# Kernel tuning notes

Hardware: AMD Instinct MI355X
Metric: run time of the kernel (lower is better)

Reference implementation:

```python
import jax, jax.numpy as jnp
import numpy as np

N_NODES = 50000
N_EDGES = 800000
F_IN = 128
HID = 32
HEADS = 8
N_CLS = 2
NEG_SLOPE = 0.2


def _segment_softmax(logits, seg, num_segments):
    # logits: [E, H], seg: [E] destination indices
    m = jax.ops.segment_max(logits, seg, num_segments=num_segments)  # [N, H]
    m = jnp.where(jnp.isfinite(m), m, 0.0)
    e = jnp.exp(logits - m[seg])
    s = jax.ops.segment_sum(e, seg, num_segments=num_segments)  # [N, H]
    return e / (s[seg] + 1e-16)


def _gat_conv(x, src, dst, W, a_src, a_dst, bias, heads, out_ch, concat):
    N = x.shape[0]
    h = (x @ W).reshape(N, heads, out_ch)           # [N, H, C]
    alpha_src = jnp.einsum('nhc,hc->nh', h, a_src)  # [N, H]
    alpha_dst = jnp.einsum('nhc,hc->nh', h, a_dst)  # [N, H]
    logits = jax.nn.leaky_relu(alpha_src[src] + alpha_dst[dst], NEG_SLOPE)  # [E, H]
    alpha = _segment_softmax(logits, dst, N)        # [E, H]
    msg = h[src] * alpha[:, :, None]                # [E, H, C]
    out = jax.ops.segment_sum(msg, dst, num_segments=N)  # [N, H, C]
    out = out.reshape(N, heads * out_ch) if concat else out.mean(axis=1)
    return out + bias


def setup_inputs() -> dict:
    key = jax.random.key(0)
    ks = jax.random.split(key, 12)
    x = jax.random.normal(ks[0], (N_NODES, F_IN), dtype=jnp.float32)
    edge_index = jax.random.randint(ks[1], (2, N_EDGES), 0, N_NODES, dtype=jnp.int32)
    batch = jnp.zeros((N_NODES,), dtype=jnp.int32)
    g1 = 1.0 / np.sqrt(F_IN)
    g2 = 1.0 / np.sqrt(HEADS * HID)
    W1 = jax.random.normal(ks[2], (F_IN, HEADS * HID), dtype=jnp.float32) * g1
    a1_src = jax.random.normal(ks[3], (HEADS, HID), dtype=jnp.float32) * g2
    a1_dst = jax.random.normal(ks[4], (HEADS, HID), dtype=jnp.float32) * g2
    b1 = jnp.zeros((HEADS * HID,), dtype=jnp.float32)
    W2 = jax.random.normal(ks[5], (HEADS * HID, N_CLS), dtype=jnp.float32) * g2
    a2_src = jax.random.normal(ks[6], (1, N_CLS), dtype=jnp.float32)
    a2_dst = jax.random.normal(ks[7], (1, N_CLS), dtype=jnp.float32)
    b2 = jnp.zeros((N_CLS,), dtype=jnp.float32)
    return {"x": x, "edge_index": edge_index, "batch": batch,
            "W1": W1, "a1_src": a1_src, "a1_dst": a1_dst, "b1": b1,
            "W2": W2, "a2_src": a2_src, "a2_dst": a2_dst, "b2": b2}


def reference(x, edge_index, batch, W1, a1_src, a1_dst, b1, W2, a2_src, a2_dst, b2):
    N = x.shape[0]
    # PyG GATConv default add_self_loops=True
    loops = jnp.arange(N, dtype=edge_index.dtype)
    src = jnp.concatenate([edge_index[0], loops])
    dst = jnp.concatenate([edge_index[1], loops])
    # dropout layers are no-ops at inference (training=False)
    h = _gat_conv(x, src, dst, W1, a1_src, a1_dst, b1, HEADS, HID, concat=True)
    h = jax.nn.elu(h)
    out = _gat_conv(h, src, dst, W2, a2_src, a2_dst, b2, 1, N_CLS, concat=False)
    return out
```

## Files before the change

kernel.cpp:

```cpp
#include <hip/hip_runtime.h>

#define NN 50000
#define NP 50048
#define NE 800000
#define ET (NE + NN)
#define NB 196
#define CAP 8192
#define EPB 4096
#define P1_B ((ET + EPB - 1) / EPB)
#define CONVW_B 32
#define CONVX_B (NP * 32 / 1024)
#define FRONT_B (P1_B + CONVW_B + CONVX_B)
#define GEMM_B (NP / 64)
#define MID_B (NB + GEMM_B)

typedef __attribute__((ext_vector_type(8))) short short8;
typedef __attribute__((ext_vector_type(4))) float f32x4;

static __device__ __forceinline__ float bf2f(unsigned short u) {
  union { unsigned int i; float f; } v; v.i = ((unsigned int)u) << 16; return v.f;
}
static __device__ __forceinline__ unsigned short f2bf(float f) {
  union { unsigned int i; float f; } v; v.f = f;
  unsigned int r = v.i + 0x7fffu + ((v.i >> 16) & 1u);
  return (unsigned short)(r >> 16);
}
static __device__ __forceinline__ float lrelu(float z) { return z > 0.f ? z : 0.2f * z; }

__global__ __launch_bounds__(1024) void k_front(
    const int* __restrict__ ei, int* __restrict__ gcount, int* __restrict__ tmp,
    const float* __restrict__ W1, unsigned short* __restrict__ wh,
    const float* __restrict__ x, unsigned short* __restrict__ xh) {
  __shared__ int hist[NB];
  __shared__ int lbase[NB];
  const int b = blockIdx.x;
  const int tid = threadIdx.x;
  if (b < P1_B) {
    if (tid < NB) hist[tid] = 0;
    __syncthreads();
    const int e0 = b * EPB + tid;
    int bkv[4], locv[4], pkv[4];
    bool val[4];
#pragma unroll
    for (int j = 0; j < 4; ++j) {
      int e = e0 + j * 1024;
      val[j] = (e < ET);
      int s = 0, d = 0;
      if (val[j]) {
        s = (e < NE) ? ei[e] : (e - NE);
        d = (e < NE) ? ei[NE + e] : (e - NE);
      }
      bkv[j] = d >> 8;
      pkv[j] = (s << 8) | (d & 255);
      locv[j] = val[j] ? atomicAdd(&hist[bkv[j]], 1) : 0;
    }
    __syncthreads();
    if (tid < NB) {
      int c = hist[tid];
      lbase[tid] = (c > 0) ? atomicAdd(&gcount[tid], c) : 0;
    }
    __syncthreads();
#pragma unroll
    for (int j = 0; j < 4; ++j)
      if (val[j]) tmp[bkv[j] * CAP + lbase[bkv[j]] + locv[j]] = pkv[j];
  } else if (b < P1_B + CONVW_B) {
    int i = (b - P1_B) * 1024 + tid;
    int k = i >> 8, n = i & 255;
    wh[n * 128 + k] = f2bf(W1[i]);
  } else {
    int i4 = (b - P1_B - CONVW_B) * 1024 + tid;
    int i = i4 * 4;
    int row = i >> 7;
    float4 v = (row < NN) ? *(const float4*)(x + i) : (float4){0.f, 0.f, 0.f, 0.f};
    ushort4 h;
    h.x = f2bf(v.x);
    h.y = f2bf(v.y);
    h.z = f2bf(v.z);
    h.w = f2bf(v.w);
    *(ushort4*)(xh + i) = h;
  }
}

__global__ __launch_bounds__(256) void k_mid(
    const int* __restrict__ tmp, const int* __restrict__ gcount,
    int* __restrict__ ssrc, int* __restrict__ row_ptr,
    const unsigned short* __restrict__ xh, const unsigned short* __restrict__ wh,
    const float* __restrict__ a1s, const float* __restrict__ a1d,
    unsigned short* __restrict__ h1, float* __restrict__ as1, float* __restrict__ ad1) {
  __shared__ unsigned short hst[64][264];
  const int tid = threadIdx.x;
  if (blockIdx.x < NB) {
    int* hist = (int*)&hst[0][0];
    int* sa = hist + 256;
    int* sb = sa + 256;
    int* cur = sb + 256;
    int* base_sh = cur + 256;
    const int t = tid;
    const int b = blockIdx.x;
    const int n_b = gcount[b];
    sa[t] = (t < NB) ? gcount[t] : 0;
    __syncthreads();
    {
      int* s = sa;
      int* d = sb;
      for (int off = 1; off < 256; off <<= 1) {
        int v = s[t];
        if (t >= off) v += s[t - off];
        d[t] = v;
        int* tm = s; s = d; d = tm;
        __syncthreads();
      }
      if (t == 0) {
        base_sh[0] = (b == 0) ? 0 : s[b - 1];
        if (b == 0) row_ptr[NN] = ET;
      }
    }
    hist[t] = 0;
    __syncthreads();
    const int base = base_sh[0];
    for (int i = t; i < n_b; i += 256) {
      int p = tmp[b * CAP + i];
      atomicAdd(&hist[p & 255], 1);
    }
    __syncthreads();
    sa[t] = hist[t];
    __syncthreads();
    {
      int* s = sa;
      int* d = sb;
      for (int off = 1; off < 256; off <<= 1) {
        int v = s[t];
        if (t >= off) v += s[t - off];
        d[t] = v;
        int* tm = s; s = d; d = tm;
        __syncthreads();
      }
      int excl = (t == 0) ? 0 : s[t - 1];
      int start = base + excl;
      cur[t] = start;
      int d_glob = (b << 8) + t;
      if (d_glob < NN) row_ptr[d_glob] = start;
    }
    __syncthreads();
    for (int i = t; i < n_b; i += 256) {
      int p = tmp[b * CAP + i];
      int pos = atomicAdd(&cur[p & 255], 1);
      ssrc[pos] = p >> 8;
    }
    return;
  }
  const int gb = blockIdx.x - NB;
  const int w = tid >> 6, lane = tid & 63;
  const int quad = lane >> 4, m16 = lane & 15;
  const int row0 = gb * 64;
  const int koff = quad * 8;

  f32x4 acc[4][4];
  for (int mt = 0; mt < 4; ++mt)
    for (int nt = 0; nt < 4; ++nt) acc[mt][nt] = (f32x4){0.f, 0.f, 0.f, 0.f};

  for (int kt = 0; kt < 4; ++kt) {
    short8 ah[4], bh[4];
    for (int mt = 0; mt < 4; ++mt) {
      size_t ra = (size_t)(row0 + mt * 16 + m16) * 128 + kt * 32 + koff;
      ah[mt] = *(const short8*)(xh + ra);
    }
    for (int nt = 0; nt < 4; ++nt) {
      size_t rb = (size_t)(w * 64 + nt * 16 + m16) * 128 + kt * 32 + koff;
      bh[nt] = *(const short8*)(wh + rb);
    }
    for (int mt = 0; mt < 4; ++mt)
      for (int nt = 0; nt < 4; ++nt)
        acc[mt][nt] = __builtin_amdgcn_mfma_f32_16x16x32_bf16(ah[mt], bh[nt], acc[mt][nt], 0, 0, 0);
  }
  for (int mt = 0; mt < 4; ++mt)
    for (int nt = 0; nt < 4; ++nt) {
      int c = w * 64 + nt * 16 + m16;
      int rb = mt * 16 + quad * 4;
      for (int r = 0; r < 4; ++r) hst[rb + r][c] = f2bf(acc[mt][nt][r]);
    }
  __syncthreads();
  for (int p = 0; p < 8; ++p) {
    int idx = p * 256 + tid;
    int row = idx >> 5, u4 = idx & 31;
    int grow = row0 + row;
    if (grow < NN) {
      uint4 v = *(const uint4*)&hst[row][u4 * 8];
      *(uint4*)(h1 + (size_t)grow * 256 + u4 * 8) = v;
    }
  }
  for (int p = 0; p < 2; ++p) {
    int id = p * 256 + tid;
    int row = id >> 3, head = id & 7;
    int grow = row0 + row;
    if (grow < NN) {
      float sa = 0.f, sd = 0.f;
      for (int c = 0; c < 32; ++c) {
        float hv = bf2f(hst[row][head * 32 + c]);
        sa = fmaf(hv, a1s[head * 32 + c], sa);
        sd = fmaf(hv, a1d[head * 32 + c], sd);
      }
      as1[(size_t)grow * 8 + head] = sa;
      ad1[(size_t)grow * 8 + head] = sd;
    }
  }
}

__global__ __launch_bounds__(256) void k_agg1(
    const int* __restrict__ row_ptr, const int* __restrict__ ssrc,
    const unsigned short* __restrict__ h1, const float* __restrict__ as1,
    const float* __restrict__ ad1, const float* __restrict__ b1,
    const float* __restrict__ W2, const float* __restrict__ a2s,
    const float* __restrict__ a2d, float4* __restrict__ nd) {
  const int lane = threadIdx.x & 63;
  const int dst = (int)((blockIdx.x * blockDim.x + threadIdx.x) >> 6);
  if (dst >= NN) return;
  const int start = row_ptr[dst], end = row_ptr[dst + 1];
  const int hA = lane & 7;
  const int eoff = lane >> 3;
  const int hB = lane >> 3;
  const int cB = (lane & 7) * 4;
  const float ad_h = ad1[(size_t)dst * 8 + hA];
  float s_loc = 0.f;
  float acc0 = 0.f, acc1 = 0.f, acc2 = 0.f, acc3 = 0.f;
  for (int base = start; base < end; base += 16) {
    int ea = base + eoff, eb = base + 8 + eoff;
    int sa_ = 0, sb_ = 0;
    float wa = 0.f, wb = 0.f;
    if (ea < end) {
      sa_ = ssrc[ea];
      wa = __expf(lrelu(as1[(size_t)sa_ * 8 + hA] + ad_h));
    }
    if (eb < end) {
      sb_ = ssrc[eb];
      wb = __expf(lrelu(as1[(size_t)sb_ * 8 + hA] + ad_h));
    }
    s_loc += wa + wb;
    uint2 u[16];
    float w16[16];
#pragma unroll
    for (int j = 0; j < 8; ++j) {
      int se = __shfl(sa_, j * 8);
      w16[j] = __shfl(wa, j * 8 + hB);
      u[j] = *(const uint2*)(h1 + (size_t)se * 256 + hB * 32 + cB);
    }
#pragma unroll
    for (int j = 0; j < 8; ++j) {
      int se = __shfl(sb_, j * 8);
      w16[8 + j] = __shfl(wb, j * 8 + hB);
      u[8 + j] = *(const uint2*)(h1 + (size_t)se * 256 + hB * 32 + cB);
    }
#pragma unroll
    for (int j = 0; j < 16; ++j) {
      float w = w16[j];
      acc0 = fmaf(w, bf2f((unsigned short)(u[j].x & 0xffffu)), acc0);
      acc1 = fmaf(w, bf2f((unsigned short)(u[j].x >> 16)), acc1);
      acc2 = fmaf(w, bf2f((unsigned short)(u[j].y & 0xffffu)), acc2);
      acc3 = fmaf(w, bf2f((unsigned short)(u[j].y >> 16)), acc3);
    }
  }
  s_loc += __shfl_xor(s_loc, 8);
  s_loc += __shfl_xor(s_loc, 16);
  s_loc += __shfl_xor(s_loc, 32);
  const float inv_s = 1.f / (s_loc + 1e-16f);
  const float inv_sB = __shfl(inv_s, hB);
  acc0 *= inv_sB; acc1 *= inv_sB; acc2 *= inv_sB; acc3 *= inv_sB;
  const int col = hB * 32 + cB;
  float av[4] = {acc0, acc1, acc2, acc3};
  float tp0 = 0.f, tp1 = 0.f;
  for (int j = 0; j < 4; ++j) {
    float v = av[j] + b1[col + j];
    v = v > 0.f ? v : (__expf(v) - 1.f);
    tp0 = fmaf(v, W2[(col + j) * 2 + 0], tp0);
    tp1 = fmaf(v, W2[(col + j) * 2 + 1], tp1);
  }
  for (int off = 32; off >= 1; off >>= 1) {
    tp0 += __shfl_xor(tp0, off);
    tp1 += __shfl_xor(tp1, off);
  }
  if (lane == 0) {
    float s2v = tp0 * a2s[0] + tp1 * a2s[1];
    float d2v = tp0 * a2d[0] + tp1 * a2d[1];
    nd[dst] = (float4){tp0, tp1, s2v, d2v};
  }
}

__global__ __launch_bounds__(256) void k_agg2(
    const int* __restrict__ row_ptr, const int* __restrict__ ssrc,
    const float4* __restrict__ nd, const float* __restrict__ b2,
    float* __restrict__ out) {
  int gid = blockIdx.x * 256 + threadIdx.x;
  int n = gid >> 3;
  int l8 = threadIdx.x & 7;
  if (n >= NN) return;
  int st = row_ptr[n], en = row_ptr[n + 1];
  float dv = nd[n].w;
  float ssum = 0.f, o0 = 0.f, o1 = 0.f;
  for (int e = st + l8; e < en; e += 8) {
    int s = ssrc[e];
    float4 v = nd[s];
    float w = __expf(lrelu(v.z + dv));
    ssum += w;
    o0 = fmaf(w, v.x, o0);
    o1 = fmaf(w, v.y, o1);
  }
  ssum += __shfl_xor(ssum, 1); o0 += __shfl_xor(o0, 1); o1 += __shfl_xor(o1, 1);
  ssum += __shfl_xor(ssum, 2); o0 += __shfl_xor(o0, 2); o1 += __shfl_xor(o1, 2);
  ssum += __shfl_xor(ssum, 4); o0 += __shfl_xor(o0, 4); o1 += __shfl_xor(o1, 4);
  if (l8 == 0) {
    float inv = 1.f / (ssum + 1e-16f);
    out[(size_t)n * 2 + 0] = o0 * inv + b2[0];
    out[(size_t)n * 2 + 1] = o1 * inv + b2[1];
  }
}

extern "C" void kernel_launch(void* const* d_in, const int* in_sizes, int n_in,
                              void* d_out, int out_size, void* d_ws, size_t ws_size,
                              hipStream_t stream) {
  const float* x = (const float*)d_in[0];
  const int* ei = (const int*)d_in[1];
  const float* W1 = (const float*)d_in[3];
  const float* a1s = (const float*)d_in[4];
  const float* a1d = (const float*)d_in[5];
  const float* b1 = (const float*)d_in[6];
  const float* W2 = (const float*)d_in[7];
  const float* a2s = (const float*)d_in[8];
  const float* a2d = (const float*)d_in[9];
  const float* b2 = (const float*)d_in[10];
  float* out = (float*)d_out;

  char* ws = (char*)d_ws;
  size_t off = 0;
  auto alloc = [&](size_t bytes) -> void* {
    void* p = ws + off;
    off += (bytes + 255) & ~(size_t)255;
    return p;
  };
  int* gcount = (int*)alloc((size_t)NB * 4);
  int* tmp = (int*)alloc((size_t)NB * CAP * 4);
  int* row_ptr = (int*)alloc((size_t)(NN + 1) * 4);
  int* ssrc = (int*)alloc((size_t)ET * 4);
  unsigned short* xh = (unsigned short*)alloc((size_t)NP * 128 * 2);
  unsigned short* wh = (unsigned short*)alloc((size_t)32768 * 2);
  unsigned short* h1 = (unsigned short*)alloc((size_t)NN * 256 * 2);
  float* as1 = (float*)alloc((size_t)NN * 8 * 4);
  float* ad1 = (float*)alloc((size_t)NN * 8 * 4);
  float4* nd = (float4*)alloc((size_t)NN * 16);
  (void)ws_size; (void)in_sizes; (void)n_in; (void)out_size;

  hipMemsetAsync(gcount, 0, (size_t)NB * 4, stream);
  k_front<<<FRONT_B, 1024, 0, stream>>>(ei, gcount, tmp, W1, wh, x, xh);
  k_mid<<<MID_B, 256, 0, stream>>>(tmp, gcount, ssrc, row_ptr, xh, wh, a1s, a1d, h1, as1, ad1);
  k_agg1<<<(NN + 3) / 4, 256, 0, stream>>>(row_ptr, ssrc, h1, as1, ad1, b1, W2, a2s, a2d, nd);
  k_agg2<<<(NN * 8 + 255) / 256, 256, 0, stream>>>(row_ptr, ssrc, nd, b2, out);
}
```

Before: 208.6 us.

## Store layer-1 features head-major and aggregate per head with atomic layer-2 projection

Layer-1 features and attention scores are now stored head-major ([head][node][32]), and layer-1 aggregation gives each block a single head. A wave processes 8 edges × 8 channel groups for one head and then atomically adds its partial layer-2 projection into a zeroed float2 buffer. The aim is a per-head gather working set small enough to stay in cache and a smaller intermediate, with the layer-2 attention scores recomputed in agg2. In exchange, row_ptr, ssrc and the edge weights are read 8 times, and the change adds global atomics, an extra memset, and non-deterministic float summation order.

After: 336.9 us. 61.6% more time.

```diff
diff --git a/kernel.cpp b/kernel.cpp
--- a/kernel.cpp
+++ b/kernel.cpp
@@ -13,6 +13,8 @@
 #define FRONT_B (P1_B + CONVW_B + CONVX_B)
 #define GEMM_B (NP / 64)
 #define MID_B (NB + GEMM_B)
+#define AGG1_GRP 1563
+#define AGG1_STRIDE (4 * AGG1_GRP)
 
 typedef __attribute__((ext_vector_type(8))) short short8;
 typedef __attribute__((ext_vector_type(4))) float f32x4;
@@ -186,7 +188,8 @@
     int grow = row0 + row;
     if (grow < NN) {
       uint4 v = *(const uint4*)&hst[row][u4 * 8];
-      *(uint4*)(h1 + (size_t)grow * 256 + u4 * 8) = v;
+      int head = u4 >> 2, cg = u4 & 3;
+      *(uint4*)(h1 + ((size_t)head * NN + grow) * 32 + cg * 8) = v;
     }
   }
   for (int p = 0; p < 2; ++p) {
@@ -200,106 +203,104 @@
         sa = fmaf(hv, a1s[head * 32 + c], sa);
         sd = fmaf(hv, a1d[head * 32 + c], sd);
       }
-      as1[(size_t)grow * 8 + head] = sa;
-      ad1[(size_t)grow * 8 + head] = sd;
+      as1[(size_t)head * NN + grow] = sa;
+      ad1[(size_t)head * NN + grow] = sd;
     }
   }
 }
 
 __global__ __launch_bounds__(256) void k_agg1(
     const int* __restrict__ row_ptr, const int* __restrict__ ssrc,
-    const unsigned short* __restrict__ h1, const float* __restrict__ as1,
-    const float* __restrict__ ad1, const float* __restrict__ b1,
-    const float* __restrict__ W2, const float* __restrict__ a2s,
-    const float* __restrict__ a2d, float4* __restrict__ nd) {
+    const unsigned short* __restrict__ h1h, const float* __restrict__ as1h,
+    const float* __restrict__ ad1h, const float* __restrict__ b1,
+    const float* __restrict__ W2, float* __restrict__ ndf) {
+  const int head = blockIdx.x & 7;
+  const int grp = blockIdx.x >> 3;
+  const int wid = threadIdx.x >> 6;
   const int lane = threadIdx.x & 63;
-  const int dst = (int)((blockIdx.x * blockDim.x + threadIdx.x) >> 6);
-  if (dst >= NN) return;
-  const int start = row_ptr[dst], end = row_ptr[dst + 1];
-  const int hA = lane & 7;
-  const int eoff = lane >> 3;
-  const int hB = lane >> 3;
-  const int cB = (lane & 7) * 4;
-  const float ad_h = ad1[(size_t)dst * 8 + hA];
-  float s_loc = 0.f;
-  float acc0 = 0.f, acc1 = 0.f, acc2 = 0.f, acc3 = 0.f;
-  for (int base = start; base < end; base += 16) {
-    int ea = base + eoff, eb = base + 8 + eoff;
-    int sa_ = 0, sb_ = 0;
-    float wa = 0.f, wb = 0.f;
-    if (ea < end) {
-      sa_ = ssrc[ea];
-      wa = __expf(lrelu(as1[(size_t)sa_ * 8 + hA] + ad_h));
-    }
-    if (eb < end) {
-      sb_ = ssrc[eb];
-      wb = __expf(lrelu(as1[(size_t)sb_ * 8 + hA] + ad_h));
-    }
-    s_loc += wa + wb;
-    uint2 u[16];
-    float w16[16];
+  const int slot = lane >> 3;
+  const int c8 = lane & 7;
+
+  const unsigned short* __restrict__ ht = h1h + (size_t)head * NN * 32;
+  const float* __restrict__ ast = as1h + (size_t)head * NN;
+  const float* __restrict__ adt = ad1h + (size_t)head * NN;
+
+  float b1c[4], w20[4], w21[4];
 #pragma unroll
-    for (int j = 0; j < 8; ++j) {
-      int se = __shfl(sa_, j * 8);
-      w16[j] = __shfl(wa, j * 8 + hB);
-      u[j] = *(const uint2*)(h1 + (size_t)se * 256 + hB * 32 + cB);
-    }
+  for (int j = 0; j < 4; ++j) {
+    int ch = head * 32 + c8 * 4 + j;
+    b1c[j] = b1[ch];
+    w20[j] = W2[ch * 2 + 0];
+    w21[j] = W2[ch * 2 + 1];
+  }
+
+  for (int dst = grp * 4 + wid; dst < NN; dst += AGG1_STRIDE) {
+    const int start = row_ptr[dst], end = row_ptr[dst + 1];
+    const float adh = adt[dst];
+    float s_loc = 0.f;
+    float a0 = 0.f, a1 = 0.f, a2 = 0.f, a3 = 0.f;
+    for (int base = start; base < end; base += 8) {
+      int e = base + slot;
+      bool v = e < end;
+      int s = v ? ssrc[e] : 0;
+      float w = 0.f;
+      if (v) w = __expf(lrelu(ast[s] + adh));
+      s_loc += w;
+      uint2 u = (uint2){0u, 0u};
+      if (v) u = *(const uint2*)(ht + (size_t)s * 32 + c8 * 4);
+      a0 = fmaf(w, bf2f((unsigned short)(u.x & 0xffffu)), a0);
+      a1 = fmaf(w, bf2f((unsigned short)(u.x >> 16)), a1);
+      a2 = fmaf(w, bf2f((unsigned short)(u.y & 0xffffu)), a2);
+      a3 = fmaf(w, bf2f((unsigned short)(u.y >> 16)), a3);
+    }
+    s_loc += __shfl_xor(s_loc, 8);
+    a0 += __shfl_xor(a0, 8); a1 += __shfl_xor(a1, 8);
+    a2 += __shfl_xor(a2, 8); a3 += __shfl_xor(a3, 8);
+    s_loc += __shfl_xor(s_loc, 16);
+    a0 += __shfl_xor(a0, 16); a1 += __shfl_xor(a1, 16);
+    a2 += __shfl_xor(a2, 16); a3 += __shfl_xor(a3, 16);
+    s_loc += __shfl_xor(s_loc, 32);
+    a0 += __shfl_xor(a0, 32); a1 += __shfl_xor(a1, 32);
+    a2 += __shfl_xor(a2, 32); a3 += __shfl_xor(a3, 32);
+    const float inv_s = 1.f / (s_loc + 1e-16f);
+    float av[4] = {a0, a1, a2, a3};
+    float tp0 = 0.f, tp1 = 0.f;
 #pragma unroll
-    for (int j = 0; j < 8; ++j) {
-      int se = __shfl(sb_, j * 8);
-      w16[8 + j] = __shfl(wb, j * 8 + hB);
-      u[8 + j] = *(const uint2*)(h1 + (size_t)se * 256 + hB * 32 + cB);
-    }
-#pragma unroll
-    for (int j = 0; j < 16; ++j) {
-      float w = w16[j];
-      acc0 = fmaf(w, bf2f((unsigned short)(u[j].x & 0xffffu)), acc0);
-      acc1 = fmaf(w, bf2f((unsigned short)(u[j].x >> 16)), acc1);
-      acc2 = fmaf(w, bf2f((unsigned short)(u[j].y & 0xffffu)), acc2);
-      acc3 = fmaf(w, bf2f((unsigned short)(u[j].y >> 16)), acc3);
-    }
-  }
-  s_loc += __shfl_xor(s_loc, 8);
-  s_loc += __shfl_xor(s_loc, 16);
-  s_loc += __shfl_xor(s_loc, 32);
-  const float inv_s = 1.f / (s_loc + 1e-16f);
-  const float inv_sB = __shfl(inv_s, hB);
-  acc0 *= inv_sB; acc1 *= inv_sB; acc2 *= inv_sB; acc3 *= inv_sB;
-  const int col = hB * 32 + cB;
-  float av[4] = {acc0, acc1, acc2, acc3};
-  float tp0 = 0.f, tp1 = 0.f;
-  for (int j = 0; j < 4; ++j) {
-    float v = av[j] + b1[col + j];
-    v = v > 0.f ? v : (__expf(v) - 1.f);
-    tp0 = fmaf(v, W2[(col + j) * 2 + 0], tp0);
-    tp1 = fmaf(v, W2[(col + j) * 2 + 1], tp1);
-  }
-  for (int off = 32; off >= 1; off >>= 1) {
-    tp0 += __shfl_xor(tp0, off);
-    tp1 += __shfl_xor(tp1, off);
-  }
-  if (lane == 0) {
-    float s2v = tp0 * a2s[0] + tp1 * a2s[1];
-    float d2v = tp0 * a2d[0] + tp1 * a2d[1];
-    nd[dst] = (float4){tp0, tp1, s2v, d2v};
+    for (int j = 0; j < 4; ++j) {
+      float vv = fmaf(av[j], inv_s, b1c[j]);
+      vv = vv > 0.f ? vv : (__expf(vv) - 1.f);
+      tp0 = fmaf(vv, w20[j], tp0);
+      tp1 = fmaf(vv, w21[j], tp1);
+    }
+    tp0 += __shfl_xor(tp0, 1); tp1 += __shfl_xor(tp1, 1);
+    tp0 += __shfl_xor(tp0, 2); tp1 += __shfl_xor(tp1, 2);
+    tp0 += __shfl_xor(tp0, 4); tp1 += __shfl_xor(tp1, 4);
+    if (lane == 0) {
+      atomicAdd(ndf + (size_t)dst * 2 + 0, tp0);
+      atomicAdd(ndf + (size_t)dst * 2 + 1, tp1);
+    }
   }
 }
 
 __global__ __launch_bounds__(256) void k_agg2(
     const int* __restrict__ row_ptr, const int* __restrict__ ssrc,
-    const float4* __restrict__ nd, const float* __restrict__ b2,
+    const float2* __restrict__ nd, const float* __restrict__ a2s,
+    const float* __restrict__ a2d, const float* __restrict__ b2,
     float* __restrict__ out) {
   int gid = blockIdx.x * 256 + threadIdx.x;
   int n = gid >> 3;
   int l8 = threadIdx.x & 7;
   if (n >= NN) return;
   int st = row_ptr[n], en = row_ptr[n + 1];
-  float dv = nd[n].w;
+  float2 td = nd[n];
+  const float s0 = a2s[0], s1 = a2s[1];
+  float dv = td.x * a2d[0] + td.y * a2d[1];
   float ssum = 0.f, o0 = 0.f, o1 = 0.f;
   for (int e = st + l8; e < en; e += 8) {
     int s = ssrc[e];
-    float4 v = nd[s];
-    float w = __expf(lrelu(v.z + dv));
+    float2 v = nd[s];
+    float zv = fmaf(v.x, s0, v.y * s1);
+    float w = __expf(lrelu(zv + dv));
     ssum += w;
     o0 = fmaf(w, v.x, o0);
     o1 = fmaf(w, v.y, o1);
@@ -345,12 +346,13 @@
   unsigned short* h1 = (unsigned short*)alloc((size_t)NN * 256 * 2);
   float* as1 = (float*)alloc((size_t)NN * 8 * 4);
   float* ad1 = (float*)alloc((size_t)NN * 8 * 4);
-  float4* nd = (float4*)alloc((size_t)NN * 16);
+  float* ndf = (float*)alloc((size_t)NN * 8);
   (void)ws_size; (void)in_sizes; (void)n_in; (void)out_size;
 
   hipMemsetAsync(gcount, 0, (size_t)NB * 4, stream);
+  hipMemsetAsync(ndf, 0, (size_t)NN * 8, stream);
   k_front<<<FRONT_B, 1024, 0, stream>>>(ei, gcount, tmp, W1, wh, x, xh);
   k_mid<<<MID_B, 256, 0, stream>>>(tmp, gcount, ssrc, row_ptr, xh, wh, a1s, a1d, h1, as1, ad1);
-  k_agg1<<<(NN + 3) / 4, 256, 0, stream>>>(row_ptr, ssrc, h1, as1, ad1, b1, W2, a2s, a2d, nd);
-  k_agg2<<<(NN * 8 + 255) / 256, 256, 0, stream>>>(row_ptr, ssrc, nd, b2, out);
-}
+  k_agg1<<<8 * AGG1_GRP, 256, 0, stream>>>(row_ptr, ssrc, h1, as1, ad1, b1, W2, ndf);
+  k_agg2<<<(NN * 8 + 255) / 256, 256, 0, stream>>>(row_ptr, ssrc, (const float2*)ndf, a2s, a2d, b2, out);
+}
```
